# Kernel tuning notes

Hardware: AMD Instinct MI355X
Metric: run time of the kernel (lower is better)

The kernel has to match this reference:

```python
import jax, jax.numpy as jnp
import numpy as np

B, N, D = 8, 128, 256
EPS = 1e-5


def _layernorm(x, g, b):
    m = jnp.mean(x, axis=-1, keepdims=True)
    v = jnp.mean(jnp.square(x - m), axis=-1, keepdims=True)
    return (x - m) * jax.lax.rsqrt(v + EPS) * g + b


def setup_inputs() -> dict:
    key = jax.random.key(0)
    ks = jax.random.split(key, 24)
    s = 0.05  # param init scale
    return {
        "text": jax.random.normal(ks[0], (B, N, D), jnp.float32),
        "adj1": jax.random.uniform(ks[1], (B, N, N), jnp.float32),
        "adj2": jax.random.uniform(ks[2], (B, N, N), jnp.float32),
        "edge1": jax.random.normal(ks[3], (B, N, N, D), jnp.float32) * 0.1,
        "edge2": jax.random.normal(ks[4], (B, N, N, D), jnp.float32) * 0.1,
        "textmask": jnp.ones((B, N), jnp.float32),
        "weight": jax.random.normal(ks[5], (D, D), jnp.float32) * s,
        "bias": jax.random.normal(ks[6], (D,), jnp.float32) * s,
        "gamma": jnp.ones((D,), jnp.float32),
        "beta": jnp.zeros((D,), jnp.float32),
        "fuse1_w": jax.random.normal(ks[7], (2 * D, D), jnp.float32) * s,
        "fuse2_w": jax.random.normal(ks[8], (2 * D, D), jnp.float32) * s,
        "fc3_w": jax.random.normal(ks[9], (2 * D, D), jnp.float32) * s,
        "fc1_w0": jax.random.normal(ks[10], (3 * D, D), jnp.float32) * s,
        "fc1_w1": jax.random.normal(ks[11], (D, 1), jnp.float32) * s,
        "fc1_b1": jnp.zeros((1,), jnp.float32),
        "fc2_w0": jax.random.normal(ks[12], (3 * D, D), jnp.float32) * s,
        "fc2_w1": jax.random.normal(ks[13], (D, 1), jnp.float32) * s,
        "fc2_b1": jnp.zeros((1,), jnp.float32),
        "align_lin": jax.random.normal(ks[14], (D, D), jnp.float32) * s,
        "align_bias": jax.random.normal(ks[15], (D,), jnp.float32) * s,
    }


def reference(text, adj1, adj2, edge1, edge2, textmask, weight, bias, gamma,
              beta, fuse1_w, fuse2_w, fc3_w, fc1_w0, fc1_w1, fc1_b1,
              fc2_w0, fc2_w1, fc2_b1, align_lin, align_bias):
    d = text.shape[-1]
    # ---- SelfAlignment ----
    logits = jnp.einsum('bid,bjd->bij', text @ align_lin, text)
    mask_add = (1.0 - textmask)[:, None, :] * -1e20
    probs = jax.nn.softmax(logits + mask_add, axis=-1)
    outss = jnp.einsum('bij,bjd->bid', probs, text) * textmask[..., None] + align_bias

    # ---- GCN body ----
    out = jax.nn.relu(text @ weight)  # [B,N,D]

    # edge contributions are loop-invariant: precompute once
    # torch cat([x,e]) @ W  ==  x @ W[:d] + e @ W[d:]
    e1_fuse = jnp.einsum('bijd,de->bije', edge1, fuse1_w[d:])
    e2_fuse = jnp.einsum('bijd,de->bije', edge2, fuse2_w[d:])
    e1_fc = jnp.einsum('bijd,de->bije', edge1, fc1_w0[2 * d:])
    e2_fc = jnp.einsum('bijd,de->bije', edge2, fc2_w0[2 * d:])

    denom1 = jnp.sum(adj1, axis=2, keepdims=True) + 1.0  # [B,N,1]
    denom2 = jnp.sum(adj2, axis=2, keepdims=True) + 1.0

    for _ in range(3):  # K = 3
        # text1[b,i,j] = out[b,i]; text2[b,i,j] = out[b,j]
        t_i1 = (out @ fc1_w0[:d])[:, :, None, :]        # text1 part, fc1
        t_j1 = (out @ fc1_w0[d:2 * d])[:, None, :, :]   # text2 part, fc1
        t_i2 = (out @ fc2_w0[:d])[:, :, None, :]
        t_j2 = (out @ fc2_w0[d:2 * d])[:, None, :, :]

        teout = jax.nn.relu((out @ fuse1_w[:d])[:, None, :, :] + e1_fuse)  # [B,N,N,D]
        tein = jax.nn.relu((out @ fuse2_w[:d])[:, None, :, :] + e2_fuse)

        s1 = jax.nn.sigmoid(jax.nn.relu(t_i1 + t_j1 + e1_fc) @ fc1_w1 + fc1_b1)[..., 0]  # [B,N,N]
        s2 = jax.nn.sigmoid(jax.nn.relu(t_i2 + t_j2 + e2_fc) @ fc2_w1 + fc2_b1)[..., 0]

        out1 = jnp.einsum('bij,bijd->bid', adj1 * s1, teout) / denom1
        out2 = jnp.einsum('bij,bijd->bid', adj2 * s2, tein) / denom2

        out = jax.nn.relu(out1 @ fc3_w[:d] + out2 @ fc3_w[d:]) + out + bias
        out = _layernorm(out, gamma, beta)  # dropout = identity (eval)
    return out, outss
```

## Files before the change

kernel.cpp:

```cpp
#include <hip/hip_runtime.h>

typedef unsigned short u16;
typedef unsigned int u32;
typedef __attribute__((ext_vector_type(8))) short bf16x8;
typedef __attribute__((ext_vector_type(4))) float f32x4;
typedef __attribute__((ext_vector_type(16))) float f32x16;

__device__ __forceinline__ u16 f2bf(float f) {
  u32 u = __float_as_uint(f);
  return (u16)((u + 0x7fffu + ((u >> 16) & 1u)) >> 16);
}
__device__ __forceinline__ float bf2f(u16 h) {
  return __uint_as_float(((u32)h) << 16);
}

__device__ __forceinline__ void glds16(const void* g, void* l) {
  __builtin_amdgcn_global_load_lds(
      (const __attribute__((address_space(1))) unsigned int*)g,
      (__attribute__((address_space(3))) unsigned int*)l, 16, 0, 0);
}

__device__ __forceinline__ f32x16 unpack16(const u16* p) {
  uint4 a = *(const uint4*)p, b = *(const uint4*)(p + 8);
  f32x16 r;
  r[0]  = __uint_as_float(a.x << 16); r[1]  = __uint_as_float(a.x & 0xffff0000u);
  r[2]  = __uint_as_float(a.y << 16); r[3]  = __uint_as_float(a.y & 0xffff0000u);
  r[4]  = __uint_as_float(a.z << 16); r[5]  = __uint_as_float(a.z & 0xffff0000u);
  r[6]  = __uint_as_float(a.w << 16); r[7]  = __uint_as_float(a.w & 0xffff0000u);
  r[8]  = __uint_as_float(b.x << 16); r[9]  = __uint_as_float(b.x & 0xffff0000u);
  r[10] = __uint_as_float(b.y << 16); r[11] = __uint_as_float(b.y & 0xffff0000u);
  r[12] = __uint_as_float(b.z << 16); r[13] = __uint_as_float(b.z & 0xffff0000u);
  r[14] = __uint_as_float(b.w << 16); r[15] = __uint_as_float(b.w & 0xffff0000u);
  return r;
}

__global__ __launch_bounds__(256) void convert_edge(
    const float* __restrict__ src, u16* __restrict__ dst) {
  int g = blockIdx.x * 256 + threadIdx.x;
  int kg = g & 7, r = (g >> 3) & 127, kc = (g >> 10) & 3, rt = g >> 12;
  const float* s = src + ((long)(rt * 128 + r) * 256 + kc * 64 + kg * 8);
  float4 a = *(const float4*)s, b = *(const float4*)(s + 4);
  ushort4 lo, hi;
  lo.x = f2bf(a.x); lo.y = f2bf(a.y); lo.z = f2bf(a.z); lo.w = f2bf(a.w);
  hi.x = f2bf(b.x); hi.y = f2bf(b.y); hi.z = f2bf(b.z); hi.w = f2bf(b.w);
  u16* d = dst + (long)rt * 65536 + kc * 16384 + r * 64 + (kg ^ (r & 7)) * 8;
  *(ushort4*)d = lo;
  *(ushort4*)(d + 4) = hi;
}

__global__ __launch_bounds__(256) void gemm_edge(
    const u16* __restrict__ A, const u16* __restrict__ Bt,
    u16* __restrict__ E) {
  __shared__ __align__(16) u16 Asm[8192];
  __shared__ __align__(16) u16 Bsm[8192];
  const int tid = threadIdx.x, lane = tid & 63, w = tid >> 6;
  const int m = lane & 15, q = lane >> 4;
  const int rt = blockIdx.x >> 2, ct = blockIdx.x & 3;
  const int wrow = (w & 1) * 64, wcol = (w >> 1) * 64;
  const char* Ab = (const char*)A + (long)rt * 131072;
  const char* Bb = (const char*)Bt + (long)ct * 65536;
  f32x4 acc[4][4];
#pragma unroll
  for (int r = 0; r < 4; ++r)
#pragma unroll
    for (int c = 0; c < 4; ++c) acc[r][c] = (f32x4){0.f, 0.f, 0.f, 0.f};

  for (int kc = 0; kc < 4; ++kc) {
#pragma unroll
    for (int t = 0; t < 4; ++t) {
      glds16(Ab + kc * 32768 + t * 4096 + tid * 16,
             (char*)Asm + t * 4096 + tid * 16);
      glds16(Bb + kc * 16384 + t * 4096 + tid * 16,
             (char*)Bsm + t * 4096 + tid * 16);
    }
    __syncthreads();
#pragma unroll
    for (int s = 0; s < 2; ++s) {
      const int ko2 = (s * 32 + q * 8) * 2;
      bf16x8 av[4], bv[4];
#pragma unroll
      for (int r = 0; r < 4; ++r) {
        int row = wrow + r * 16 + m;
        av[r] = *(const bf16x8*)((const char*)Asm + row * 128 +
                                 (ko2 ^ ((row & 7) * 16)));
      }
#pragma unroll
      for (int c = 0; c < 4; ++c) {
        int col = wcol + c * 16 + m;
        bv[c] = *(const bf16x8*)((const char*)Bsm + col * 128 +
                                 (ko2 ^ ((col & 7) * 16)));
      }
#pragma unroll
      for (int r = 0; r < 4; ++r)
#pragma unroll
        for (int c = 0; c < 4; ++c)
          acc[r][c] = __builtin_amdgcn_mfma_f32_16x16x32_bf16(
              av[r], bv[c], acc[r][c], 0, 0, 0);
    }
    __syncthreads();
  }
#pragma unroll
  for (int r = 0; r < 4; ++r)
#pragma unroll
    for (int c = 0; c < 4; ++c)
#pragma unroll
      for (int g = 0; g < 4; ++g) {
        long gr = (long)rt * 128 + wrow + r * 16 + q * 4 + g;
        int gc = ct * 128 + wcol + c * 16 + m;
        E[gr * 512 + gc] = f2bf(acc[r][c][g]);
      }
}

template<int K, int ROWS, bool OUT_BF16>
__global__ __launch_bounds__(256) void gemm_mfma(
    const float* __restrict__ A, const u16* __restrict__ Bt,
    void* __restrict__ Cv, int Ntot) {
  constexpr int LD = 72;
  constexpr int CF = (ROWS == 128) ? 8 : 4;
  __shared__ __align__(16) u16 Asm[ROWS * LD];
  __shared__ __align__(16) u16 Bsm[256 * LD];
  const int tid = threadIdx.x;
  const int lane = tid & 63;
  const int w = tid >> 6;
  const int m = lane & 15;
  const int q = lane >> 4;
  const int wrow = (ROWS == 128) ? (w & 1) * 64 : 0;
  const int wcol = (ROWS == 128) ? (w >> 1) * 128 : w * 64;
  const long rowbase = (long)blockIdx.x * ROWS;
  const long colbase = (long)blockIdx.y * 256;
  f32x4 acc[4][CF];
#pragma unroll
  for (int r = 0; r < 4; ++r)
#pragma unroll
    for (int c = 0; c < CF; ++c) acc[r][c] = (f32x4){0.f, 0.f, 0.f, 0.f};

  for (int kc = 0; kc < K / 64; ++kc) {
    const int kb = kc * 64;
#pragma unroll
    for (int it = 0; it < ROWS / 16; ++it) {
      int f = it * 256 + tid;
      int r = f >> 4, c4 = (f & 15) * 4;
      float4 v = *(const float4*)(A + (rowbase + r) * K + kb + c4);
      ushort4 h;
      h.x = f2bf(v.x); h.y = f2bf(v.y); h.z = f2bf(v.z); h.w = f2bf(v.w);
      *(ushort4*)&Asm[r * LD + c4] = h;
    }
#pragma unroll
    for (int it = 0; it < 8; ++it) {
      int f = it * 256 + tid;
      int c = f >> 3, k8 = (f & 7) * 8;
      *(uint4*)&Bsm[c * LD + k8] =
          *(const uint4*)(Bt + (colbase + c) * K + kb + k8);
    }
    __syncthreads();
#pragma unroll
    for (int s = 0; s < 2; ++s) {
      const int ko = s * 32 + q * 8;
      bf16x8 av[4], bv[CF];
#pragma unroll
      for (int r = 0; r < 4; ++r)
        av[r] = *(const bf16x8*)&Asm[(wrow + r * 16 + m) * LD + ko];
#pragma unroll
      for (int c = 0; c < CF; ++c)
        bv[c] = *(const bf16x8*)&Bsm[(wcol + c * 16 + m) * LD + ko];
#pragma unroll
      for (int r = 0; r < 4; ++r)
#pragma unroll
        for (int c = 0; c < CF; ++c)
          acc[r][c] = __builtin_amdgcn_mfma_f32_16x16x32_bf16(
              av[r], bv[c], acc[r][c], 0, 0, 0);
    }
    __syncthreads();
  }
#pragma unroll
  for (int r = 0; r < 4; ++r)
#pragma unroll
    for (int c = 0; c < CF; ++c)
#pragma unroll
      for (int g = 0; g < 4; ++g) {
        long gr = rowbase + wrow + r * 16 + q * 4 + g;
        long gc = colbase + wcol + c * 16 + m;
        float v = acc[r][c][g];
        if (OUT_BF16) ((u16*)Cv)[gr * Ntot + gc] = f2bf(v);
        else          ((float*)Cv)[gr * Ntot + gc] = v;
      }
}

__global__ __launch_bounds__(256) void prep_bt(
    const float* __restrict__ weight, const float* __restrict__ align_lin,
    const float* __restrict__ fuse1_w, const float* __restrict__ fuse2_w,
    const float* __restrict__ fc1_w0, const float* __restrict__ fc2_w0,
    const float* __restrict__ fc3_w,
    u16* BtE1, u16* BtE2, u16* BtW0, u16* BtLoop, u16* BtFc3) {
  int g = blockIdx.x * 256 + threadIdx.x;
  if (g < 262144) {
    int t = g & 131071;
    int col = t >> 8, k = t & 255;
    float v;
    if (g < 131072)
      v = (col < 256) ? fuse1_w[(256 + k) * 256 + col]
                      : fc1_w0[(512 + k) * 256 + (col - 256)];
    else
      v = (col < 256) ? fuse2_w[(256 + k) * 256 + col]
                      : fc2_w0[(512 + k) * 256 + (col - 256)];
    int ct = col >> 7, cc = col & 127, kc = k >> 6, kk = k & 63;
    u16* dst = (g < 131072) ? BtE1 : BtE2;
    dst[ct * 32768 + kc * 8192 + cc * 64 + (kk ^ ((cc & 7) * 8))] = f2bf(v);
  } else if (g < 393216) {
    int t = g - 262144;
    int c = t >> 8, k = t & 255;
    float v = (c < 256) ? weight[k * 256 + c] : align_lin[k * 256 + (c - 256)];
    BtW0[t] = f2bf(v);
  } else if (g < 786432) {
    int t = g - 393216;
    int c = t >> 8, k = t & 255;
    int seg = c >> 8, cc = c & 255;
    float v;
    if      (seg == 0) v = fuse1_w[k * 256 + cc];
    else if (seg == 1) v = fuse2_w[k * 256 + cc];
    else if (seg == 2) v = fc1_w0[k * 256 + cc];
    else if (seg == 3) v = fc1_w0[(256 + k) * 256 + cc];
    else if (seg == 4) v = fc2_w0[k * 256 + cc];
    else               v = fc2_w0[(256 + k) * 256 + cc];
    BtLoop[t] = f2bf(v);
  } else {
    int t = g - 786432;
    int c = t >> 9, k = t & 511;
    BtFc3[t] = f2bf(fc3_w[k * 256 + c]);
  }
}

__global__ __launch_bounds__(256) void relu0_kernel(const float* __restrict__ T0,
                                                    float* __restrict__ outb) {
  long r = blockIdx.x;
  int d = threadIdx.x;
  outb[r * 256 + d] = fmaxf(T0[r * 512 + d], 0.f);
}

__global__ __launch_bounds__(128) void align_kernel(
    const float* __restrict__ text, const float* __restrict__ T0,
    const float* __restrict__ textmask, const float* __restrict__ align_bias,
    float* __restrict__ outss) {
  const int bi = blockIdx.x;
  const int b = bi >> 7;
  const int tid = threadIdx.x;
  __shared__ float ta[256];
  __shared__ float pr[128];
  __shared__ float red[128];
  ta[tid]       = T0[(long)bi * 512 + 256 + tid];
  ta[tid + 128] = T0[(long)bi * 512 + 384 + tid];
  __syncthreads();
  const float* trow = text + (long)(b * 128 + tid) * 256;
  float dot = 0.f;
  for (int d = 0; d < 256; d += 4) {
    float4 t4 = *(const float4*)(trow + d);
    dot += t4.x * ta[d] + t4.y * ta[d + 1] + t4.z * ta[d + 2] + t4.w * ta[d + 3];
  }
  float logit = dot + (1.0f - textmask[b * 128 + tid]) * -1e20f;
  pr[tid] = logit;
  red[tid] = logit;
  __syncthreads();
  for (int off = 64; off; off >>= 1) {
    if (tid < off) red[tid] = fmaxf(red[tid], red[tid + off]);
    __syncthreads();
  }
  float mx = red[0];
  __syncthreads();
  float e = __expf(pr[tid] - mx);
  red[tid] = e;
  __syncthreads();
  for (int off = 64; off; off >>= 1) {
    if (tid < off) red[tid] += red[tid + off];
    __syncthreads();
  }
  float inv = 1.0f / red[0];
  __syncthreads();
  pr[tid] = e * inv;
  __syncthreads();
  const float mi = textmask[bi];
  for (int h = 0; h < 2; ++h) {
    int d = tid + h * 128;
    float s = 0.f;
    for (int j = 0; j < 128; ++j)
      s += pr[j] * text[(long)(b * 128 + j) * 256 + d];
    outss[(long)bi * 256 + d] = s * mi + align_bias[d];
  }
}

__global__ __launch_bounds__(256) void fused_gate(
    const u16* __restrict__ E1, const u16* __restrict__ E2,
    const float* __restrict__ P, const float* __restrict__ adj1,
    const float* __restrict__ adj2, const float* __restrict__ fc1w1,
    const float* __restrict__ fc1b1, const float* __restrict__ fc2w1,
    const float* __restrict__ fc2b1, float* __restrict__ OU12) {
  const int tid = threadIdx.x, lane = tid & 63, w = tid >> 6;
  const int g16 = lane >> 4, l16 = lane & 15;
  const int bi = blockIdx.x, b = bi >> 7;
  const int db = l16 * 16;
  const long rowi = (long)bi * 1536;
  const f32x16 w1v = *(const f32x16*)(fc1w1 + db);
  const f32x16 w2v = *(const f32x16*)(fc2w1 + db);
  const f32x16 ti1 = *(const f32x16*)(P + rowi + 512 + db);
  const f32x16 ti2 = *(const f32x16*)(P + rowi + 1024 + db);
  const float b1 = fc1b1[0], b2 = fc2b1[0];
  const long ebase = (long)bi * 65536;
  const int abase = bi * 128;
  f32x16 acc1, acc2;
#pragma unroll
  for (int dd = 0; dd < 16; ++dd) { acc1[dd] = 0.f; acc2[dd] = 0.f; }
  float da1 = 0.f, da2 = 0.f;

  for (int t = 0; t < 8; ++t) {
    const int j = w * 32 + t * 4 + g16;
    const long er = ebase + (long)j * 512;
    const long rowj = (long)(b * 128 + j) * 1536;
    f32x16 e1cf = unpack16(E1 + er + 256 + db);
    f32x16 e2cf = unpack16(E2 + er + 256 + db);
    f32x16 tj1 = *(const f32x16*)(P + rowj + 768 + db);
    f32x16 tj2 = *(const f32x16*)(P + rowj + 1280 + db);
    float a1 = adj1[abase + j], a2 = adj2[abase + j];
    float z1 = 0.f, z2 = 0.f;
#pragma unroll
    for (int dd = 0; dd < 16; ++dd) {
      z1 += fmaxf(ti1[dd] + tj1[dd] + e1cf[dd], 0.f) * w1v[dd];
      z2 += fmaxf(ti2[dd] + tj2[dd] + e2cf[dd], 0.f) * w2v[dd];
    }
#pragma unroll
    for (int off = 1; off < 16; off <<= 1) {
      z1 += __shfl_xor(z1, off);
      z2 += __shfl_xor(z2, off);
    }
    float s1 = a1 / (1.f + __expf(-(z1 + b1)));
    float s2 = a2 / (1.f + __expf(-(z2 + b2)));
    f32x16 e1ff = unpack16(E1 + er + db);
    f32x16 e2ff = unpack16(E2 + er + db);
    f32x16 of1 = *(const f32x16*)(P + rowj + db);
    f32x16 of2 = *(const f32x16*)(P + rowj + 256 + db);
#pragma unroll
    for (int dd = 0; dd < 16; ++dd) {
      acc1[dd] += s1 * fmaxf(of1[dd] + e1ff[dd], 0.f);
      acc2[dd] += s2 * fmaxf(of2[dd] + e2ff[dd], 0.f);
    }
    da1 += a1;
    da2 += a2;
  }

  __shared__ float redA[16][260];
  __shared__ float redB[16][260];
  __shared__ float dA[16], dB[16];
  const int p = w * 4 + g16;
#pragma unroll
  for (int v = 0; v < 4; ++v) {
    *(float4*)&redA[p][db + v * 4] =
        make_float4(acc1[v*4], acc1[v*4+1], acc1[v*4+2], acc1[v*4+3]);
    *(float4*)&redB[p][db + v * 4] =
        make_float4(acc2[v*4], acc2[v*4+1], acc2[v*4+2], acc2[v*4+3]);
  }
  if (l16 == 0) { dA[p] = da1; dB[p] = da2; }
  __syncthreads();
  float o1 = 0.f, o2 = 0.f, d1 = 1.f, d2 = 1.f;
#pragma unroll
  for (int pp = 0; pp < 16; ++pp) {
    o1 += redA[pp][tid];
    o2 += redB[pp][tid];
    d1 += dA[pp];
    d2 += dB[pp];
  }
  OU12[(long)bi * 512 + tid] = o1 / d1;
  OU12[(long)bi * 512 + 256 + tid] = o2 / d2;
}

__global__ __launch_bounds__(256) void ln_kernel(
    const float* __restrict__ Y, const float* __restrict__ prev,
    const float* __restrict__ bias, const float* __restrict__ gamma,
    const float* __restrict__ beta, float* __restrict__ dst) {
  const int row = blockIdx.x, tid = threadIdx.x, lane = tid & 63, w = tid >> 6;
  const long idx = (long)row * 256 + tid;
  float v = fmaxf(Y[idx], 0.f) + prev[idx] + bias[tid];
  float s = v;
#pragma unroll
  for (int off = 32; off; off >>= 1) s += __shfl_xor(s, off);
  __shared__ float wsA[4], wsB[4];
  if (lane == 0) wsA[w] = s;
  __syncthreads();
  float mean = (wsA[0] + wsA[1] + wsA[2] + wsA[3]) * (1.0f / 256.0f);
  float c = v - mean;
  float s2 = c * c;
#pragma unroll
  for (int off = 32; off; off >>= 1) s2 += __shfl_xor(s2, off);
  if (lane == 0) wsB[w] = s2;
  __syncthreads();
  float var = (wsB[0] + wsB[1] + wsB[2] + wsB[3]) * (1.0f / 256.0f);
  dst[idx] = c * rsqrtf(var + 1e-5f) * gamma[tid] + beta[tid];
}

extern "C" void kernel_launch(void* const* d_in, const int* in_sizes, int n_in,
                              void* d_out, int out_size, void* d_ws, size_t ws_size,
                              hipStream_t stream) {
  const float* text      = (const float*)d_in[0];
  const float* adj1      = (const float*)d_in[1];
  const float* adj2      = (const float*)d_in[2];
  const float* edge1     = (const float*)d_in[3];
  const float* edge2     = (const float*)d_in[4];
  const float* textmask  = (const float*)d_in[5];
  const float* weight    = (const float*)d_in[6];
  const float* bias      = (const float*)d_in[7];
  const float* gamma     = (const float*)d_in[8];
  const float* beta      = (const float*)d_in[9];
  const float* fuse1_w   = (const float*)d_in[10];
  const float* fuse2_w   = (const float*)d_in[11];
  const float* fc3_w     = (const float*)d_in[12];
  const float* fc1_w0    = (const float*)d_in[13];
  const float* fc1_w1    = (const float*)d_in[14];
  const float* fc1_b1    = (const float*)d_in[15];
  const float* fc2_w0    = (const float*)d_in[16];
  const float* fc2_w1    = (const float*)d_in[17];
  const float* fc2_b1    = (const float*)d_in[18];
  const float* align_lin = (const float*)d_in[19];
  const float* align_bias= (const float*)d_in[20];
  float* outF = (float*)d_out;

  char* w8 = (char*)d_ws;
  u16* Ax   = (u16*)w8;
  u16* E1   = (u16*)(w8 + 67108864);
  u16* E2   = (u16*)(w8 + 201326592);
  u16* BtE1 = (u16*)(w8 + 335544320);
  u16* BtE2 = BtE1 + 131072;
  u16* BtW0 = BtE2 + 131072;
  u16* BtLoop = BtW0 + 131072;
  u16* BtFc3  = BtLoop + 393216;
  float* P    = (float*)w8;
  float* T0   = P + 1572864;
  float* OU12 = T0 + 524288;
  float* outb = OU12 + 524288;
  float* Yb   = outb + 262144;

  prep_bt<<<3584, 256, 0, stream>>>(weight, align_lin, fuse1_w, fuse2_w,
                                    fc1_w0, fc2_w0, fc3_w,
                                    BtE1, BtE2, BtW0, BtLoop, BtFc3);
  convert_edge<<<16384, 256, 0, stream>>>(edge1, Ax);
  gemm_edge<<<4096, 256, 0, stream>>>(Ax, BtE1, E1);
  convert_edge<<<16384, 256, 0, stream>>>(edge2, Ax);
  gemm_edge<<<4096, 256, 0, stream>>>(Ax, BtE2, E2);
  gemm_mfma<256, 64, false><<<dim3(16, 2), 256, 0, stream>>>(text, BtW0, T0, 512);
  relu0_kernel<<<1024, 256, 0, stream>>>(T0, outb);
  align_kernel<<<1024, 128, 0, stream>>>(text, T0, textmask, align_bias,
                                         outF + 262144);
  for (int it = 0; it < 3; ++it) {
    gemm_mfma<256, 64, false><<<dim3(16, 6), 256, 0, stream>>>(outb, BtLoop, P, 1536);
    fused_gate<<<1024, 256, 0, stream>>>(E1, E2, P, adj1, adj2, fc1_w1, fc1_b1,
                                         fc2_w1, fc2_b1, OU12);
    gemm_mfma<512, 64, false><<<dim3(16, 1), 256, 0, stream>>>(OU12, BtFc3, Yb, 256);
    ln_kernel<<<1024, 256, 0, stream>>>(Yb, outb, bias, gamma, beta,
                                        (it == 2) ? outF : outb);
  }
}
```

Before: 764.2 us.

## Split fused_gate over j-chunks, swizzle edge GEMM blocks, fuse relu0, nontemporal edge convert

fused_gate now runs 4096 blocks of 128 threads, each covering a quarter of the j range, and a new merge_ou kernel sums the partial results and divides by the denominators. This is meant to raise occupancy and parallelism in the main loop, at the cost of an extra launch and a round trip of partials through global memory. gemm_edge remaps block indices so each XCD works on adjacent row tiles, and convert_edge uses nontemporal 16-byte loads and stores. The initial GEMM now writes the relu output and the align projection directly, which removes relu0_kernel. align_kernel uses 256 threads so each thread computes one output column.

```diff
diff --git a/kernel.cpp b/kernel.cpp
--- a/kernel.cpp
+++ b/kernel.cpp
@@ -5,13 +5,11 @@
 typedef __attribute__((ext_vector_type(8))) short bf16x8;
 typedef __attribute__((ext_vector_type(4))) float f32x4;
 typedef __attribute__((ext_vector_type(16))) float f32x16;
+typedef __attribute__((ext_vector_type(8))) u16 u16x8;
 
 __device__ __forceinline__ u16 f2bf(float f) {
   u32 u = __float_as_uint(f);
   return (u16)((u + 0x7fffu + ((u >> 16) & 1u)) >> 16);
-}
-__device__ __forceinline__ float bf2f(u16 h) {
-  return __uint_as_float(((u32)h) << 16);
 }
 
 __device__ __forceinline__ void glds16(const void* g, void* l) {
@@ -39,13 +37,13 @@
   int g = blockIdx.x * 256 + threadIdx.x;
   int kg = g & 7, r = (g >> 3) & 127, kc = (g >> 10) & 3, rt = g >> 12;
   const float* s = src + ((long)(rt * 128 + r) * 256 + kc * 64 + kg * 8);
-  float4 a = *(const float4*)s, b = *(const float4*)(s + 4);
-  ushort4 lo, hi;
-  lo.x = f2bf(a.x); lo.y = f2bf(a.y); lo.z = f2bf(a.z); lo.w = f2bf(a.w);
-  hi.x = f2bf(b.x); hi.y = f2bf(b.y); hi.z = f2bf(b.z); hi.w = f2bf(b.w);
+  f32x4 a = __builtin_nontemporal_load((const f32x4*)s);
+  f32x4 b = __builtin_nontemporal_load((const f32x4*)(s + 4));
+  u16x8 h;
+  h[0] = f2bf(a[0]); h[1] = f2bf(a[1]); h[2] = f2bf(a[2]); h[3] = f2bf(a[3]);
+  h[4] = f2bf(b[0]); h[5] = f2bf(b[1]); h[6] = f2bf(b[2]); h[7] = f2bf(b[3]);
   u16* d = dst + (long)rt * 65536 + kc * 16384 + r * 64 + (kg ^ (r & 7)) * 8;
-  *(ushort4*)d = lo;
-  *(ushort4*)(d + 4) = hi;
+  __builtin_nontemporal_store(h, (u16x8*)d);
 }
 
 __global__ __launch_bounds__(256) void gemm_edge(
@@ -55,7 +53,10 @@
   __shared__ __align__(16) u16 Bsm[8192];
   const int tid = threadIdx.x, lane = tid & 63, w = tid >> 6;
   const int m = lane & 15, q = lane >> 4;
-  const int rt = blockIdx.x >> 2, ct = blockIdx.x & 3;
+  const int p = blockIdx.x;
+  const int sidx = p >> 3, xcd = p & 7;
+  const int rt = (sidx >> 2) * 8 + xcd;
+  const int ct = sidx & 3;
   const int wrow = (w & 1) * 64, wcol = (w >> 1) * 64;
   const char* Ab = (const char*)A + (long)rt * 131072;
   const char* Bb = (const char*)Bt + (long)ct * 65536;
@@ -111,33 +112,31 @@
       }
 }
 
-template<int K, int ROWS, bool OUT_BF16>
+template<int K, int MODE>
 __global__ __launch_bounds__(256) void gemm_mfma(
     const float* __restrict__ A, const u16* __restrict__ Bt,
-    void* __restrict__ Cv, int Ntot) {
+    void* __restrict__ Cv, float* __restrict__ C2, int Ntot) {
   constexpr int LD = 72;
-  constexpr int CF = (ROWS == 128) ? 8 : 4;
-  __shared__ __align__(16) u16 Asm[ROWS * LD];
+  __shared__ __align__(16) u16 Asm[64 * LD];
   __shared__ __align__(16) u16 Bsm[256 * LD];
   const int tid = threadIdx.x;
   const int lane = tid & 63;
   const int w = tid >> 6;
   const int m = lane & 15;
   const int q = lane >> 4;
-  const int wrow = (ROWS == 128) ? (w & 1) * 64 : 0;
-  const int wcol = (ROWS == 128) ? (w >> 1) * 128 : w * 64;
-  const long rowbase = (long)blockIdx.x * ROWS;
+  const int wcol = w * 64;
+  const long rowbase = (long)blockIdx.x * 64;
   const long colbase = (long)blockIdx.y * 256;
-  f32x4 acc[4][CF];
+  f32x4 acc[4][4];
 #pragma unroll
   for (int r = 0; r < 4; ++r)
 #pragma unroll
-    for (int c = 0; c < CF; ++c) acc[r][c] = (f32x4){0.f, 0.f, 0.f, 0.f};
+    for (int c = 0; c < 4; ++c) acc[r][c] = (f32x4){0.f, 0.f, 0.f, 0.f};
 
   for (int kc = 0; kc < K / 64; ++kc) {
     const int kb = kc * 64;
 #pragma unroll
-    for (int it = 0; it < ROWS / 16; ++it) {
+    for (int it = 0; it < 4; ++it) {
       int f = it * 256 + tid;
       int r = f >> 4, c4 = (f & 15) * 4;
       float4 v = *(const float4*)(A + (rowbase + r) * K + kb + c4);
@@ -156,17 +155,17 @@
 #pragma unroll
     for (int s = 0; s < 2; ++s) {
       const int ko = s * 32 + q * 8;
-      bf16x8 av[4], bv[CF];
+      bf16x8 av[4], bv[4];
 #pragma unroll
       for (int r = 0; r < 4; ++r)
-        av[r] = *(const bf16x8*)&Asm[(wrow + r * 16 + m) * LD + ko];
-#pragma unroll
-      for (int c = 0; c < CF; ++c)
+        av[r] = *(const bf16x8*)&Asm[(r * 16 + m) * LD + ko];
+#pragma unroll
+      for (int c = 0; c < 4; ++c)
         bv[c] = *(const bf16x8*)&Bsm[(wcol + c * 16 + m) * LD + ko];
 #pragma unroll
       for (int r = 0; r < 4; ++r)
 #pragma unroll
-        for (int c = 0; c < CF; ++c)
+        for (int c = 0; c < 4; ++c)
           acc[r][c] = __builtin_amdgcn_mfma_f32_16x16x32_bf16(
               av[r], bv[c], acc[r][c], 0, 0, 0);
     }
@@ -175,14 +174,18 @@
 #pragma unroll
   for (int r = 0; r < 4; ++r)
 #pragma unroll
-    for (int c = 0; c < CF; ++c)
+    for (int c = 0; c < 4; ++c)
 #pragma unroll
       for (int g = 0; g < 4; ++g) {
-        long gr = rowbase + wrow + r * 16 + q * 4 + g;
+        long gr = rowbase + r * 16 + q * 4 + g;
         long gc = colbase + wcol + c * 16 + m;
         float v = acc[r][c][g];
-        if (OUT_BF16) ((u16*)Cv)[gr * Ntot + gc] = f2bf(v);
-        else          ((float*)Cv)[gr * Ntot + gc] = v;
+        if (MODE == 1)      ((u16*)Cv)[gr * Ntot + gc] = f2bf(v);
+        else if (MODE == 0) ((float*)Cv)[gr * Ntot + gc] = v;
+        else {
+          if (gc < 256) ((float*)Cv)[gr * 256 + gc] = fmaxf(v, 0.f);
+          else          C2[gr * 256 + gc - 256] = v;
+        }
       }
 }
 
@@ -230,15 +233,8 @@
   }
 }
 
-__global__ __launch_bounds__(256) void relu0_kernel(const float* __restrict__ T0,
-                                                    float* __restrict__ outb) {
-  long r = blockIdx.x;
-  int d = threadIdx.x;
-  outb[r * 256 + d] = fmaxf(T0[r * 512 + d], 0.f);
-}
-
-__global__ __launch_bounds__(128) void align_kernel(
-    const float* __restrict__ text, const float* __restrict__ T0,
+__global__ __launch_bounds__(256) void align_kernel(
+    const float* __restrict__ text, const float* __restrict__ Ta,
     const float* __restrict__ textmask, const float* __restrict__ align_bias,
     float* __restrict__ outss) {
   const int bi = blockIdx.x;
@@ -247,18 +243,20 @@
   __shared__ float ta[256];
   __shared__ float pr[128];
   __shared__ float red[128];
-  ta[tid]       = T0[(long)bi * 512 + 256 + tid];
-  ta[tid + 128] = T0[(long)bi * 512 + 384 + tid];
-  __syncthreads();
-  const float* trow = text + (long)(b * 128 + tid) * 256;
-  float dot = 0.f;
-  for (int d = 0; d < 256; d += 4) {
-    float4 t4 = *(const float4*)(trow + d);
-    dot += t4.x * ta[d] + t4.y * ta[d + 1] + t4.z * ta[d + 2] + t4.w * ta[d + 3];
-  }
-  float logit = dot + (1.0f - textmask[b * 128 + tid]) * -1e20f;
-  pr[tid] = logit;
-  red[tid] = logit;
+  ta[tid] = Ta[(long)bi * 256 + tid];
+  __syncthreads();
+  float e = 0.f;
+  if (tid < 128) {
+    const float* trow = text + (long)(b * 128 + tid) * 256;
+    float dot = 0.f;
+    for (int d = 0; d < 256; d += 4) {
+      float4 t4 = *(const float4*)(trow + d);
+      dot += t4.x * ta[d] + t4.y * ta[d + 1] + t4.z * ta[d + 2] + t4.w * ta[d + 3];
+    }
+    float logit = dot + (1.0f - textmask[b * 128 + tid]) * -1e20f;
+    pr[tid] = logit;
+    red[tid] = logit;
+  }
   __syncthreads();
   for (int off = 64; off; off >>= 1) {
     if (tid < off) red[tid] = fmaxf(red[tid], red[tid + off]);
@@ -266,8 +264,10 @@
   }
   float mx = red[0];
   __syncthreads();
-  float e = __expf(pr[tid] - mx);
-  red[tid] = e;
+  if (tid < 128) {
+    e = __expf(pr[tid] - mx);
+    red[tid] = e;
+  }
   __syncthreads();
   for (int off = 64; off; off >>= 1) {
     if (tid < off) red[tid] += red[tid + off];
@@ -275,27 +275,28 @@
   }
   float inv = 1.0f / red[0];
   __syncthreads();
-  pr[tid] = e * inv;
+  if (tid < 128) pr[tid] = e * inv;
   __syncthreads();
   const float mi = textmask[bi];
-  for (int h = 0; h < 2; ++h) {
-    int d = tid + h * 128;
-    float s = 0.f;
-    for (int j = 0; j < 128; ++j)
-      s += pr[j] * text[(long)(b * 128 + j) * 256 + d];
-    outss[(long)bi * 256 + d] = s * mi + align_bias[d];
-  }
-}
-
-__global__ __launch_bounds__(256) void fused_gate(
+  float s = 0.f;
+  const float* tcol = text + (long)b * 32768 + tid;
+#pragma unroll 4
+  for (int j = 0; j < 128; ++j) s += pr[j] * tcol[j * 256];
+  outss[(long)bi * 256 + tid] = s * mi + align_bias[tid];
+}
+
+__global__ __launch_bounds__(128, 4) void fused_gate(
     const u16* __restrict__ E1, const u16* __restrict__ E2,
     const float* __restrict__ P, const float* __restrict__ adj1,
     const float* __restrict__ adj2, const float* __restrict__ fc1w1,
     const float* __restrict__ fc1b1, const float* __restrict__ fc2w1,
-    const float* __restrict__ fc2b1, float* __restrict__ OU12) {
+    const float* __restrict__ fc2b1, float* __restrict__ OUP,
+    float* __restrict__ DAP) {
   const int tid = threadIdx.x, lane = tid & 63, w = tid >> 6;
   const int g16 = lane >> 4, l16 = lane & 15;
-  const int bi = blockIdx.x, b = bi >> 7;
+  const int blk = blockIdx.x;
+  const int bi = blk >> 2, jc = blk & 3;
+  const int b = bi >> 7;
   const int db = l16 * 16;
   const long rowi = (long)bi * 1536;
   const f32x16 w1v = *(const f32x16*)(fc1w1 + db);
@@ -310,8 +311,9 @@
   for (int dd = 0; dd < 16; ++dd) { acc1[dd] = 0.f; acc2[dd] = 0.f; }
   float da1 = 0.f, da2 = 0.f;
 
-  for (int t = 0; t < 8; ++t) {
-    const int j = w * 32 + t * 4 + g16;
+#pragma unroll 2
+  for (int t = 0; t < 4; ++t) {
+    const int j = jc * 32 + w * 16 + t * 4 + g16;
     const long er = ebase + (long)j * 512;
     const long rowj = (long)(b * 128 + j) * 1536;
     f32x16 e1cf = unpack16(E1 + er + 256 + db);
@@ -345,29 +347,54 @@
     da2 += a2;
   }
 
-  __shared__ float redA[16][260];
-  __shared__ float redB[16][260];
-  __shared__ float dA[16], dB[16];
-  const int p = w * 4 + g16;
+  __shared__ float redA[8][260];
+  __shared__ float redB[8][260];
+  __shared__ float dA[8], dB[8];
+  const int pidx = w * 4 + g16;
 #pragma unroll
   for (int v = 0; v < 4; ++v) {
-    *(float4*)&redA[p][db + v * 4] =
+    *(float4*)&redA[pidx][db + v * 4] =
         make_float4(acc1[v*4], acc1[v*4+1], acc1[v*4+2], acc1[v*4+3]);
-    *(float4*)&redB[p][db + v * 4] =
+    *(float4*)&redB[pidx][db + v * 4] =
         make_float4(acc2[v*4], acc2[v*4+1], acc2[v*4+2], acc2[v*4+3]);
   }
-  if (l16 == 0) { dA[p] = da1; dB[p] = da2; }
-  __syncthreads();
-  float o1 = 0.f, o2 = 0.f, d1 = 1.f, d2 = 1.f;
-#pragma unroll
-  for (int pp = 0; pp < 16; ++pp) {
-    o1 += redA[pp][tid];
-    o2 += redB[pp][tid];
-    d1 += dA[pp];
-    d2 += dB[pp];
-  }
-  OU12[(long)bi * 512 + tid] = o1 / d1;
-  OU12[(long)bi * 512 + 256 + tid] = o2 / d2;
+  if (l16 == 0) { dA[pidx] = da1; dB[pidx] = da2; }
+  __syncthreads();
+#pragma unroll
+  for (int h = 0; h < 2; ++h) {
+    int col = h * 128 + tid;
+    float o1 = 0.f, o2 = 0.f;
+#pragma unroll
+    for (int pp = 0; pp < 8; ++pp) {
+      o1 += redA[pp][col];
+      o2 += redB[pp][col];
+    }
+    OUP[(long)blk * 512 + col] = o1;
+    OUP[(long)blk * 512 + 256 + col] = o2;
+  }
+  if (tid == 0) {
+    float d1 = 0.f, d2 = 0.f;
+#pragma unroll
+    for (int pp = 0; pp < 8; ++pp) { d1 += dA[pp]; d2 += dB[pp]; }
+    DAP[blk * 2] = d1;
+    DAP[blk * 2 + 1] = d2;
+  }
+}
+
+__global__ __launch_bounds__(256) void merge_ou(
+    const float* __restrict__ OUP, const float* __restrict__ DAP,
+    float* __restrict__ OU12) {
+  const int bi = blockIdx.x, tid = threadIdx.x;
+  const long base = (long)bi * 4 * 512;
+  float d1 = 1.f + DAP[bi*8+0] + DAP[bi*8+2] + DAP[bi*8+4] + DAP[bi*8+6];
+  float d2 = 1.f + DAP[bi*8+1] + DAP[bi*8+3] + DAP[bi*8+5] + DAP[bi*8+7];
+#pragma unroll
+  for (int h = 0; h < 2; ++h) {
+    int col = h * 256 + tid;
+    float o = OUP[base + col] + OUP[base + 512 + col] +
+              OUP[base + 1024 + col] + OUP[base + 1536 + col];
+    OU12[(long)bi * 512 + col] = o / ((col < 256) ? d1 : d2);
+  }
 }
 
 __global__ __launch_bounds__(256) void ln_kernel(
@@ -430,10 +457,12 @@
   u16* BtLoop = BtW0 + 131072;
   u16* BtFc3  = BtLoop + 393216;
   float* P    = (float*)w8;
-  float* T0   = P + 1572864;
-  float* OU12 = T0 + 524288;
+  float* Ta   = P + 1572864;
+  float* OU12 = Ta + 262144;
   float* outb = OU12 + 524288;
   float* Yb   = outb + 262144;
+  float* OUP  = Yb + 262144;
+  float* DAP  = OUP + 2097152;
 
   prep_bt<<<3584, 256, 0, stream>>>(weight, align_lin, fuse1_w, fuse2_w,
                                     fc1_w0, fc2_w0, fc3_w,
@@ -442,15 +471,15 @@
   gemm_edge<<<4096, 256, 0, stream>>>(Ax, BtE1, E1);
   convert_edge<<<16384, 256, 0, stream>>>(edge2, Ax);
   gemm_edge<<<4096, 256, 0, stream>>>(Ax, BtE2, E2);
-  gemm_mfma<256, 64, false><<<dim3(16, 2), 256, 0, stream>>>(text, BtW0, T0, 512);
-  relu0_kernel<<<1024, 256, 0, stream>>>(T0, outb);
-  align_kernel<<<1024, 128, 0, stream>>>(text, T0, textmask, align_bias,
+  gemm_mfma<256, 2><<<dim3(16, 2), 256, 0, stream>>>(text, BtW0, outb, Ta, 512);
+  align_kernel<<<1024, 256, 0, stream>>>(text, Ta, textmask, align_bias,
                                          outF + 262144);
   for (int it = 0; it < 3; ++it) {
-    gemm_mfma<256, 64, false><<<dim3(16, 6), 256, 0, stream>>>(outb, BtLoop, P, 1536);
-    fused_gate<<<1024, 256, 0, stream>>>(E1, E2, P, adj1, adj2, fc1_w1, fc1_b1,
-                                         fc2_w1, fc2_b1, OU12);
-    gemm_mfma<512, 64, false><<<dim3(16, 1), 256, 0, stream>>>(OU12, BtFc3, Yb, 256);
+    gemm_mfma<256, 0><<<dim3(16, 6), 256, 0, stream>>>(outb, BtLoop, P, nullptr, 1536);
+    fused_gate<<<4096, 128, 0, stream>>>(E1, E2, P, adj1, adj2, fc1_w1, fc1_b1,
+                                         fc2_w1, fc2_b1, OUP, DAP);
+    merge_ou<<<1024, 256, 0, stream>>>(OUP, DAP, OU12);
+    gemm_mfma<512, 0><<<dim3(16, 1), 256, 0, stream>>>(OU12, BtFc3, Yb, nullptr, 256);
     ln_kernel<<<1024, 256, 0, stream>>>(Yb, outb, bias, gamma, beta,
                                         (it == 2) ? outF : outb);
   }
```

New measurement: 1.322 ms. 73.0% more time.
